# Optimization experiments

Measured on AMD Instinct MI355X. Metric: run time of the kernel, lower is better.

## Reference

```python
import jax, jax.numpy as jnp
import numpy as np

EPS = 1e-5
NEIGHBOR_K = 3
NEG_SLOPE = 0.2

def _conv(x, w):
    # x: [N,C,H,W], w: [O,I,3,3], stride 1, SAME padding
    return jax.lax.conv_general_dilated(
        x, w, window_strides=(1, 1), padding='SAME',
        dimension_numbers=('NCHW', 'OIHW', 'NCHW'))

def _bn(x, gamma, beta):
    # BatchNorm2d in training mode: batch statistics over (N,H,W), biased var
    m = x.mean(axis=(0, 2, 3), keepdims=True)
    v = x.var(axis=(0, 2, 3), keepdims=True)
    xn = (x - m) * jax.lax.rsqrt(v + EPS)
    return xn * gamma.reshape(1, -1, 1, 1) + beta.reshape(1, -1, 1, 1)

def _lrelu(x):
    return jnp.where(x >= 0, x, NEG_SLOPE * x)

def _maxpool2(x):
    return jax.lax.reduce_window(x, -jnp.inf, jax.lax.max,
                                 (1, 1, 2, 2), (1, 1, 2, 2), 'VALID')

def _features(x, w1, g1, b1, w2, g2, b2, w3, g3, b3, w4, g4, b4):
    x = _maxpool2(_lrelu(_bn(_conv(x, w1), g1, b1)))
    x = _maxpool2(_lrelu(_bn(_conv(x, w2), g2, b2)))
    x = _lrelu(_bn(_conv(x, w3), g3, b3))
    x = _lrelu(_bn(_conv(x, w4), g4, b4))
    return x  # [N, 64, 21, 21]

def setup_inputs() -> dict:
    key = jax.random.key(0)
    ks = jax.random.split(key, 8)
    inp = {
        'input1': jax.random.normal(ks[0], (32, 3, 84, 84), jnp.float32),
        'input2': jax.random.normal(ks[1], (5, 5, 3, 84, 84), jnp.float32),
        'w1': jax.random.normal(ks[2], (64, 3, 3, 3), jnp.float32) * 0.1,
        'g1': jax.random.uniform(ks[3], (64,), jnp.float32, 0.5, 1.5),
        'b1': jnp.zeros((64,), jnp.float32),
        'w2': jax.random.normal(ks[4], (64, 64, 3, 3), jnp.float32) * 0.1,
        'g2': jax.random.uniform(ks[5], (64,), jnp.float32, 0.5, 1.5),
        'b2': jnp.zeros((64,), jnp.float32),
        'w3': jax.random.normal(ks[6], (64, 64, 3, 3), jnp.float32) * 0.1,
        'g3': jax.random.uniform(ks[7], (64,), jnp.float32, 0.5, 1.5),
        'b3': jnp.zeros((64,), jnp.float32),
        'w4': jax.random.normal(jax.random.fold_in(key, 100), (64, 64, 3, 3), jnp.float32) * 0.1,
        'g4': jax.random.uniform(jax.random.fold_in(key, 101), (64,), jnp.float32, 0.5, 1.5),
        'b4': jnp.zeros((64,), jnp.float32),
    }
    return inp

def reference(input1, input2, w1, g1, b1, w2, g2, b2, w3, g3, b3, w4, g4, b4):
    params = (w1, g1, b1, w2, g2, b2, w3, g3, b3, w4, g4, b4)
    # Query features: [B, C, h, w]
    q = _features(input1, *params)
    B, C, h, w = q.shape
    hw = h * w
    Q = q.reshape(B, C, hw).transpose(0, 2, 1)            # [B, hw, C]
    qn = jnp.linalg.norm(Q, axis=2, keepdims=True)        # [B, hw, 1]
    # Support features, BN stats per class-batch (matches per-class forward)
    s = jax.vmap(lambda x: _features(x, *params))(input2) # [nc, shot, C, h, w]
    nc, shot = s.shape[0], s.shape[1]
    S = s.transpose(0, 2, 1, 3, 4).reshape(nc, C, shot * hw)  # [nc, C, M]
    sn = jnp.linalg.norm(S, axis=1, keepdims=True)            # [nc, 1, M]
    # Cosine similarities: [B, nc, hw, M]
    sims = jnp.einsum('bqc,ncm->bnqm', Q, S)
    sims = sims / (qn[:, None, :, :] * sn[None, :, :, :])
    topv = jax.lax.top_k(sims, NEIGHBOR_K)[0]              # [B, nc, hw, k]
    return topv.sum(axis=(2, 3))                           # [B, nc]
```

## Files before the change

kernel.cpp:

```cpp
#include <hip/hip_runtime.h>
#include <hip/hip_bf16.h>
#include <stdint.h>

#define NQ 32
#define NCLS 5
#define SHOT 5
#define NIMG 57
#define P1 7056
#define P2 1764
#define P3 441
#define PX 3528
#define MM (SHOT*P3)
#define EPSB 1e-5f
#define SLOPE 0.2f
#define NEGINF -3.4e38f
#define NREP 32
#define MSPAN 576
#define MRNG 4
#define SLS 88

typedef __attribute__((ext_vector_type(8))) short short8;
typedef __attribute__((ext_vector_type(4))) float f32x4;

__device__ inline float ldf(const float* p) { return *p; }
__device__ inline float ldf(const __hip_bfloat16* p) { return __bfloat162float(*p); }
__device__ inline void stf(float* p, float v) { *p = v; }
__device__ inline void stf(__hip_bfloat16* p, float v) { *p = __float2bfloat16(v); }

__device__ __forceinline__ unsigned short bf16bits(float v)
{
    __hip_bfloat16 h = __float2bfloat16(v);
    return *reinterpret_cast<unsigned short*>(&h);
}
__device__ __forceinline__ float bits2f(unsigned short u)
{
    unsigned int x = ((unsigned int)u) << 16;
    return *reinterpret_cast<float*>(&x);
}

__global__ void pack_all_k(const float* __restrict__ w1, const float* __restrict__ w2,
                           const float* __restrict__ w3, const float* __restrict__ w4,
                           unsigned short* __restrict__ wpk1, unsigned short* __restrict__ wpk2,
                           unsigned short* __restrict__ wpk3, unsigned short* __restrict__ wpk4,
                           float* __restrict__ sums)
{
    int i = blockIdx.x * 256 + threadIdx.x;
    if (i < 4 * 6 * 64 * 2 * NREP) sums[i] = 0.f;
    if (i < 3 * 36864) {
        int set = i / 36864, ii = i - set * 36864;
        const float* w = (set == 0) ? w2 : (set == 1) ? w3 : w4;
        unsigned short* wpk = (set == 0) ? wpk2 : (set == 1) ? wpk3 : wpk4;
        int j = ii & 7, lane = (ii >> 3) & 63, chunk = ii >> 9;
        int nt = chunk & 3, half = (chunk >> 2) & 1, t = chunk >> 3;
        int co = nt * 16 + (lane & 15);
        int ci = half * 32 + (lane >> 4) * 8 + j;
        wpk[ii] = bf16bits(w[co * 576 + ci * 9 + t]);
    } else {
        int ii = i - 3 * 36864;
        if (ii >= 4096) return;
        int j = ii & 7, lane = (ii >> 3) & 63, c8 = ii >> 9;
        int nt = c8 & 3, f = c8 >> 2;
        int co = nt * 16 + (lane & 15), q = lane >> 4;
        int k = q * 8 + j;
        float val = 0.f;
        if (f == 0) {
            int t = k >> 2, ci = k & 3;
            if (ci < 3) val = w1[co * 27 + ci * 9 + t];
        } else if (k < 4) {
            int ci = k & 3;
            if (ci < 3) val = w1[co * 27 + ci * 9 + 8];
        }
        wpk1[ii] = bf16bits(val);
    }
}

__global__ __launch_bounds__(256) void conv1m_k(const float* __restrict__ in1,
                                                const float* __restrict__ in2,
                                                const unsigned short* __restrict__ wpk1,
                                                __hip_bfloat16* __restrict__ xpool,
                                                float* __restrict__ sums)
{
    constexpr int S = 84, P = P1, MBLK = 256, NB = 28, SPAN = MBLK + 2 * S + 2;
    __shared__ __align__(16) unsigned short ls4[SPAN * 4];
    __shared__ float qs[4][64], qs2[4][64];
    int img = blockIdx.x / NB;
    int p0 = (blockIdx.x % NB) * MBLK;
    int tid = threadIdx.x, lane = tid & 63, wv = tid >> 6;
    int col = lane & 15, quad = lane >> 4;
    const float* in = (img < NQ) ? in1 + (size_t)img * 3 * P1
                                 : in2 + (size_t)(img - NQ) * 3 * P1;
    for (int u = tid; u < SPAN; u += 256) {
        int p = p0 - S - 1 + u;
        union { unsigned short us[4]; uint2 u2; } o;
        o.u2 = (uint2){0u, 0u};
        if (p >= 0 && p < P) {
            o.us[0] = bf16bits(in[p]);
            o.us[1] = bf16bits(in[P1 + p]);
            o.us[2] = bf16bits(in[2 * P1 + p]);
        }
        *(uint2*)(ls4 + u * 4) = o.u2;
    }
    const short8* wb = (const short8*)wpk1;
    short8 b0[4], b1[4];
    #pragma unroll
    for (int nt = 0; nt < 4; ++nt) {
        b0[nt] = wb[(size_t)(nt * 64 + lane)];
        b1[nt] = wb[(size_t)((4 + nt) * 64 + lane)];
    }
    int t0 = 2 * quad, t1 = t0 + 1;
    int d0 = (t0 / 3 - 1) * S + (t0 % 3 - 1);
    int d1 = (t1 / 3 - 1) * S + (t1 % 3 - 1);
    const int d8 = S + 1;
    int tx0 = t0 % 3, tx1 = t1 % 3;
    __syncthreads();
    f32x4 acc[4][4];
    #pragma unroll
    for (int mt = 0; mt < 4; ++mt)
        #pragma unroll
        for (int nt = 0; nt < 4; ++nt) acc[mt][nt] = (f32x4){0.f, 0.f, 0.f, 0.f};
    #pragma unroll
    for (int mt = 0; mt < 4; ++mt) {
        int pl = wv * 64 + mt * 16 + col;
        int xm = (p0 + pl) % S;
        int base = pl + S + 1;
        uint2 h0 = *(const uint2*)(ls4 + (base + d0) * 4);
        uint2 h1 = *(const uint2*)(ls4 + (base + d1) * 4);
        uint2 h8 = *(const uint2*)(ls4 + (base + d8) * 4);
        bool ok0 = (tx0 == 0) ? (xm >= 1) : ((tx0 == 2) ? (xm <= S - 2) : true);
        bool ok1 = (tx1 == 0) ? (xm >= 1) : ((tx1 == 2) ? (xm <= S - 2) : true);
        bool ok8 = (quad == 0) && (xm <= S - 2);
        if (!ok0) h0 = (uint2){0u, 0u};
        if (!ok1) h1 = (uint2){0u, 0u};
        if (!ok8) h8 = (uint2){0u, 0u};
        union { uint4 u; short8 s; } ca, cb;
        ca.u = (uint4){h0.x, h0.y, h1.x, h1.y};
        cb.u = (uint4){h8.x, h8.y, 0u, 0u};
        #pragma unroll
        for (int nt = 0; nt < 4; ++nt) {
            acc[mt][nt] = __builtin_amdgcn_mfma_f32_16x16x32_bf16(ca.s, b0[nt], acc[mt][nt], 0, 0, 0);
            acc[mt][nt] = __builtin_amdgcn_mfma_f32_16x16x32_bf16(cb.s, b1[nt], acc[mt][nt], 0, 0, 0);
        }
    }
    float s[4] = {0.f, 0.f, 0.f, 0.f}, s2[4] = {0.f, 0.f, 0.f, 0.f};
    __hip_bfloat16* ob = xpool + (size_t)img * PX * 64;
    #pragma unroll
    for (int mt = 0; mt < 4; ++mt) {
        int tb = p0 + wv * 64 + mt * 16 + quad * 4;
        #pragma unroll
        for (int reg = 0; reg < 4; ++reg) {
            int pr = tb + reg;
            if (pr < P) {
                #pragma unroll
                for (int nt = 0; nt < 4; ++nt) {
                    float v = acc[mt][nt][reg];
                    s[nt] += v;
                    s2[nt] = fmaf(v, v, s2[nt]);
                }
            }
        }
        #pragma unroll
        for (int pr2 = 0; pr2 < 2; ++pr2) {
            int m0 = tb + pr2 * 2;
            if (m0 < P) {
                #pragma unroll
                for (int nt = 0; nt < 4; ++nt) {
                    float v = fmaxf(acc[mt][nt][pr2 * 2], acc[mt][nt][pr2 * 2 + 1]);
                    ob[(size_t)(m0 >> 1) * 64 + nt * 16 + col] = __float2bfloat16(v);
                }
            }
        }
    }
    #pragma unroll
    for (int d = 16; d < 64; d <<= 1)
        #pragma unroll
        for (int nt = 0; nt < 4; ++nt) {
            s[nt] += __shfl_xor(s[nt], d, 64);
            s2[nt] += __shfl_xor(s2[nt], d, 64);
        }
    if (quad == 0) {
        #pragma unroll
        for (int nt = 0; nt < 4; ++nt) {
            qs[wv][nt * 16 + col] = s[nt];
            qs2[wv][nt * 16 + col] = s2[nt];
        }
    }
    __syncthreads();
    if (wv == 0) {
        int g = (img < NQ) ? 0 : 1 + (img - NQ) / SHOT;
        int rep = blockIdx.x & (NREP - 1);
        float ts = qs[0][lane] + qs[1][lane] + qs[2][lane] + qs[3][lane];
        float ts2 = qs2[0][lane] + qs2[1][lane] + qs2[2][lane] + qs2[3][lane];
        float* base = sums + ((size_t)(g * 64 + lane) * 2) * NREP + rep;
        atomicAdd(base, ts);
        atomicAdd(base + NREP, ts2);
    }
}

__global__ __launch_bounds__(256) void bnpooly_k(const unsigned short* __restrict__ in,
                                                 const float* __restrict__ ms,
                                                 unsigned short* __restrict__ out)
{
    int i = blockIdx.x * 256 + threadIdx.x;
    if (i >= NIMG * P2 * 16) return;
    int q4 = i & 15;
    int t = i >> 4;
    int p = t % P2;
    int img = t / P2;
    int y = p / 42, x2 = p - y * 42;
    int g = (img < NQ) ? 0 : 1 + (img - NQ) / SHOT;
    size_t base = ((size_t)img * PX + (size_t)(2 * y) * 42 + x2) * 16 + q4;
    ushort4 r0 = ((const ushort4*)in)[base];
    ushort4 r1 = ((const ushort4*)in)[base + 42 * 16];
    unsigned short a0[4] = {r0.x, r0.y, r0.z, r0.w};
    unsigned short a1[4] = {r1.x, r1.y, r1.z, r1.w};
    ushort4 o;
    unsigned short* os = (unsigned short*)&o;
    #pragma unroll
    for (int k = 0; k < 4; ++k) {
        int c = q4 * 4 + k;
        float v = fmaxf(bits2f(a0[k]), bits2f(a1[k]));
        v = fmaf(v, ms[(g * 64 + c) * 2], ms[(g * 64 + c) * 2 + 1]);
        v = fmaxf(v, SLOPE * v);
        os[k] = bf16bits(v);
    }
    ((ushort4*)out)[i] = o;
}

template <int S, int MBLK, bool BNIN, typename OT>
__global__ __launch_bounds__(256) void conv64m_k(const void* __restrict__ inv,
                                                 const unsigned short* __restrict__ wpk,
                                                 OT* __restrict__ out,
                                                 float* __restrict__ sums,
                                                 const float* __restrict__ msin)
{
    constexpr int P = S * S;
    constexpr int MT = MBLK / 64;
    constexpr int NB = (P + MBLK - 1) / MBLK;
    constexpr int SPAN = MBLK + 2 * S + 2;
    __shared__ __align__(16) unsigned short ls[SPAN * 72];
    __shared__ float qs[4][64], qs2[4][64];
    int img = blockIdx.x / NB;
    int p0 = (blockIdx.x % NB) * MBLK;
    int tid = threadIdx.x;
    int lane = tid & 63, wv = tid >> 6;
    int col = lane & 15, quad = lane >> 4;
    int g = (img < NQ) ? 0 : 1 + (img - NQ) / SHOT;
    if constexpr (!BNIN) {
        const unsigned short* ib = (const unsigned short*)inv + (size_t)img * P * 64;
        for (int u = tid; u < SPAN * 8; u += 256) {
            int pix = u >> 3, part = u & 7;
            int p = p0 - S - 1 + pix;
            short8 v = {0, 0, 0, 0, 0, 0, 0, 0};
            if (p >= 0 && p < P) v = *(const short8*)(ib + (size_t)p * 64 + part * 8);
            *(short8*)(ls + pix * 72 + part * 8) = v;
        }
    } else {
        const float* ib = (const float*)inv + (size_t)img * P * 64;
        int part = tid & 7;
        float ba[8], bb[8];
        #pragma unroll
        for (int j = 0; j < 8; ++j) {
            float2 ab = ((const float2*)msin)[g * 64 + part * 8 + j];
            ba[j] = ab.x;
            bb[j] = ab.y;
        }
        for (int u = tid; u < SPAN * 8; u += 256) {
            int pix = u >> 3;
            int p = p0 - S - 1 + pix;
            union { unsigned short us[8]; short8 s8; } o;
            #pragma unroll
            for (int j = 0; j < 8; ++j) o.us[j] = 0;
            if (p >= 0 && p < P) {
                const float* src = ib + (size_t)p * 64 + part * 8;
                float4 x0 = *(const float4*)src;
                float4 x1 = *(const float4*)(src + 4);
                float xs[8] = {x0.x, x0.y, x0.z, x0.w, x1.x, x1.y, x1.z, x1.w};
                #pragma unroll
                for (int j = 0; j < 8; ++j) {
                    float v = fmaf(xs[j], ba[j], bb[j]);
                    v = fmaxf(v, SLOPE * v);
                    o.us[j] = bf16bits(v);
                }
            }
            *(short8*)(ls + pix * 72 + part * 8) = o.s8;
        }
    }
    __syncthreads();
    f32x4 acc[MT][4];
    #pragma unroll
    for (int mt = 0; mt < MT; ++mt)
        #pragma unroll
        for (int nt = 0; nt < 4; ++nt) acc[mt][nt] = (f32x4){0.f, 0.f, 0.f, 0.f};
    bool mok0[MT], mok2[MT];
    #pragma unroll
    for (int mt = 0; mt < MT; ++mt) {
        int xm = (p0 + wv * (MT * 16) + mt * 16 + col) % S;
        mok0[mt] = xm >= 1;
        mok2[mt] = xm <= S - 2;
    }
    const short8* wb = (const short8*)wpk;
    #pragma unroll
    for (int ky = 0; ky < 3; ++ky) {
        #pragma unroll
        for (int kx = 0; kx < 3; ++kx) {
            int t = ky * 3 + kx;
            int d = (ky - 1) * S + (kx - 1);
            #pragma unroll
            for (int half = 0; half < 2; ++half) {
                short8 b[4];
                #pragma unroll
                for (int nt = 0; nt < 4; ++nt)
                    b[nt] = wb[((t * 2 + half) * 4 + nt) * 64 + lane];
                #pragma unroll
                for (int mt = 0; mt < MT; ++mt) {
                    int idx = wv * (MT * 16) + mt * 16 + col + S + 1 + d;
                    short8 a = *(const short8*)(ls + idx * 72 + half * 32 + quad * 8);
                    bool ok = (kx == 0) ? mok0[mt] : (kx == 2) ? mok2[mt] : true;
                    if (!ok) a = (short8){0, 0, 0, 0, 0, 0, 0, 0};
                    #pragma unroll
                    for (int nt = 0; nt < 4; ++nt)
                        acc[mt][nt] = __builtin_amdgcn_mfma_f32_16x16x32_bf16(a, b[nt], acc[mt][nt], 0, 0, 0);
                }
            }
        }
    }
    float s[4] = {0.f, 0.f, 0.f, 0.f}, s2[4] = {0.f, 0.f, 0.f, 0.f};
    OT* ob = out + (size_t)img * P * 64;
    #pragma unroll
    for (int mt = 0; mt < MT; ++mt) {
        int tb = p0 + wv * (MT * 16) + mt * 16 + quad * 4;
        #pragma unroll
        for (int reg = 0; reg < 4; ++reg) {
            int pr = tb + reg;
            if (pr < P) {
                #pragma unroll
                for (int nt = 0; nt < 4; ++nt) {
                    float v = acc[mt][nt][reg];
                    stf(ob + (size_t)pr * 64 + nt * 16 + col, v);
                    s[nt] += v;
                    s2[nt] = fmaf(v, v, s2[nt]);
                }
            }
        }
    }
    #pragma unroll
    for (int d = 16; d < 64; d <<= 1)
        #pragma unroll
        for (int nt = 0; nt < 4; ++nt) {
            s[nt] += __shfl_xor(s[nt], d, 64);
            s2[nt] += __shfl_xor(s2[nt], d, 64);
        }
    if (quad == 0) {
        #pragma unroll
        for (int nt = 0; nt < 4; ++nt) {
            qs[wv][nt * 16 + col] = s[nt];
            qs2[wv][nt * 16 + col] = s2[nt];
        }
    }
    __syncthreads();
    if (wv == 0) {
        int rep = blockIdx.x & (NREP - 1);
        float ts = qs[0][lane] + qs[1][lane] + qs[2][lane] + qs[3][lane];
        float ts2 = qs2[0][lane] + qs2[1][lane] + qs2[2][lane] + qs2[3][lane];
        float* base = sums + ((size_t)(g * 64 + lane) * 2) * NREP + rep;
        atomicAdd(base, ts);
        atomicAdd(base + NREP, ts2);
    }
}

__global__ void finalize_k(const float* __restrict__ sums, float* __restrict__ ms,
                           const float* __restrict__ gamma, const float* __restrict__ beta, int P)
{
    int i = blockIdx.x * blockDim.x + threadIdx.x;
    if (i >= 6 * 64) return;
    int g = i >> 6, c = i & 63;
    const float* ps = sums + (size_t)i * 2 * NREP;
    float s = 0.f, s2 = 0.f;
    #pragma unroll
    for (int r = 0; r < NREP; ++r) { s += ps[r]; s2 += ps[NREP + r]; }
    float cnt = (float)((g == 0 ? NQ : SHOT) * P);
    float mean = s / cnt;
    float var = s2 / cnt - mean * mean;
    float a = rsqrtf(var + EPSB) * gamma[c];
    ms[i * 2] = a;
    ms[i * 2 + 1] = fmaf(-mean, a, beta[c]);
}

template <typename T>
__global__ __launch_bounds__(256) void bnpool_k(const T* __restrict__ x, const float* __restrict__ ms,
                                                __hip_bfloat16* __restrict__ out, int Win)
{
    int Wout = Win >> 1, Pout = Wout * Wout;
    size_t idx = (size_t)blockIdx.x * 256 + threadIdx.x;
    size_t total = (size_t)NIMG * Pout * 64;
    if (idx >= total) return;
    int c = (int)(idx & 63);
    size_t t = idx >> 6;
    int p = (int)(t % Pout);
    int img = (int)(t / Pout);
    int y = p / Wout, xo = p - y * Wout;
    int g = (img < NQ) ? 0 : 1 + (img - NQ) / SHOT;
    float a = ms[(g * 64 + c) * 2], bb = ms[(g * 64 + c) * 2 + 1];
    const T* base = x + (((size_t)img * Win + 2 * y) * Win + 2 * xo) * 64 + c;
    float mx = -3.4e38f;
    #pragma unroll
    for (int dy = 0; dy < 2; ++dy)
        #pragma unroll
        for (int dx = 0; dx < 2; ++dx) {
            float v = ldf(base + ((size_t)dy * Win + dx) * 64);
            v = fmaf(v, a, bb);
            v = v >= 0.f ? v : SLOPE * v;
            mx = fmaxf(mx, v);
        }
    out[idx] = __float2bfloat16(mx);
}

__global__ __launch_bounds__(256) void bnnorm_k(const float* __restrict__ x, const float* __restrict__ ms,
                                                __hip_bfloat16* __restrict__ out)
{
    int lane = threadIdx.x & 63, wvr = threadIdx.x >> 6;
    int pix = blockIdx.x * 4 + wvr;
    if (pix >= NIMG * P3) return;
    int img = pix / P3;
    int g = (img < NQ) ? 0 : 1 + (img - NQ) / SHOT;
    float v = fmaf(x[(size_t)pix * 64 + lane], ms[(g * 64 + lane) * 2], ms[(g * 64 + lane) * 2 + 1]);
    v = v >= 0.f ? v : SLOPE * v;
    float ss = v * v;
    #pragma unroll
    for (int d = 32; d > 0; d >>= 1) ss += __shfl_xor(ss, d, 64);
    out[(size_t)pix * 64 + lane] = __float2bfloat16(v * rsqrtf(ss));
}

__device__ __forceinline__ void ins3(float v, float& t0, float& t1, float& t2)
{
    float n1 = __builtin_amdgcn_fmed3f(v, t0, t1);
    float n2 = __builtin_amdgcn_fmed3f(v, t1, t2);
    t0 = fmaxf(t0, v);
    t1 = n1;
    t2 = n2;
}

__global__ __launch_bounds__(256, 6) void sim_part_k(const __hip_bfloat16* __restrict__ fhat,
                                                     float* __restrict__ part)
{
    __shared__ __align__(16) unsigned short sl[64 * SLS];
    int t = blockIdx.x;
    int mr = t & 3;
    int qb = (t >> 2) % 7;
    int n = (t / 28) % NCLS;
    int bq = t / (28 * NCLS);
    int tid = threadIdx.x, lane = tid & 63, wv = tid >> 6;
    int col = lane & 15, quad = lane >> 4;
    int q = qb * 64 + wv * 16 + col;
    int qc = q < P3 ? q : P3 - 1;
    const unsigned short* qp = (const unsigned short*)fhat + ((size_t)bq * P3 + qc) * 64;
    short8 a0 = *(const short8*)(qp + quad * 8);
    short8 a1 = *(const short8*)(qp + 32 + quad * 8);
    const unsigned short* sp = (const unsigned short*)fhat + (size_t)(NQ + n * SHOT) * P3 * 64;
    int m_lo = mr * MSPAN;
    int m_cnt = MM - m_lo; if (m_cnt > MSPAN) m_cnt = MSPAN;
    int nch = (m_cnt + 63) >> 6;
    float t0[4], t1[4], t2[4];
    #pragma unroll
    for (int r = 0; r < 4; ++r) { t0[r] = NEGINF; t1[r] = NEGINF; t2[r] = NEGINF; }
    int srow = tid >> 3, scc = (tid & 7) * 8;
    for (int c = 0; c < nch; ++c) {
        int m0 = m_lo + c * 64;
        __syncthreads();
        #pragma unroll
        for (int pass = 0; pass < 2; ++pass) {
            int row = srow + pass * 32;
            int m = m0 + row;
            short8 vv = {0, 0, 0, 0, 0, 0, 0, 0};
            if (m < MM) vv = *(const short8*)(sp + (size_t)m * 64 + scc);
            *(short8*)(sl + row * SLS + scc) = vv;
        }
        __syncthreads();
        const unsigned short* sr = sl + col * SLS + quad * 8;
        #pragma unroll
        for (int mt = 0; mt < 4; ++mt) {
            if (m0 + mt * 16 < MM) {
                short8 b0 = *(const short8*)(sr);
                short8 b1 = *(const short8*)(sr + 32);
                f32x4 acc = {0.f, 0.f, 0.f, 0.f};
                acc = __builtin_amdgcn_mfma_f32_16x16x32_bf16(a0, b0, acc, 0, 0, 0);
                acc = __builtin_amdgcn_mfma_f32_16x16x32_bf16(a1, b1, acc, 0, 0, 0);
                #pragma unroll
                for (int r = 0; r < 4; ++r) ins3(acc[r], t0[r], t1[r], t2[r]);
            }
            sr += 16 * SLS;
        }
    }
    #pragma unroll
    for (int d = 1; d < 16; d <<= 1)
        #pragma unroll
        for (int r = 0; r < 4; ++r) {
            float u0 = __shfl_xor(t0[r], d, 64);
            float u1 = __shfl_xor(t1[r], d, 64);
            float u2 = __shfl_xor(t2[r], d, 64);
            ins3(u0, t0[r], t1[r], t2[r]);
            ins3(u1, t0[r], t1[r], t2[r]);
            ins3(u2, t0[r], t1[r], t2[r]);
        }
    if (col == 0) {
        #pragma unroll
        for (int r = 0; r < 4; ++r) {
            int ql = wv * 16 + quad * 4 + r;
            float* pp = part + ((((size_t)(bq * NCLS + n) * 7 + qb) * 4 + mr) * 64 + ql) * 3;
            pp[0] = t0[r];
            pp[1] = t1[r];
            pp[2] = t2[r];
        }
    }
}

__global__ __launch_bounds__(256) void sim_merge_k(const float* __restrict__ part,
                                                   float* __restrict__ out)
{
    __shared__ float red[4];
    int b = blockIdx.x;
    int tid = threadIdx.x, lane = tid & 63, wv = tid >> 6;
    float s = 0.f;
    for (int q = tid; q < P3; q += 256) {
        int qb = q >> 6, ql = q & 63;
        const float* pp = part + (((size_t)b * 7 + qb) * 4 * 64 + ql) * 3;
        float v0 = pp[0], v1 = pp[1], v2 = pp[2];
        #pragma unroll
        for (int mr = 1; mr < 4; ++mr) {
            const float* pm = pp + (size_t)mr * 192;
            ins3(pm[0], v0, v1, v2);
            ins3(pm[1], v0, v1, v2);
            ins3(pm[2], v0, v1, v2);
        }
        s += v0 + v1 + v2;
    }
    #pragma unroll
    for (int d = 32; d > 0; d >>= 1) s += __shfl_xor(s, d, 64);
    if (lane == 0) red[wv] = s;
    __syncthreads();
    if (tid == 0) out[b] = red[0] + red[1] + red[2] + red[3];
}

extern "C" void kernel_launch(void* const* d_in, const int* in_sizes, int n_in,
                              void* d_out, int out_size, void* d_ws, size_t ws_size,
                              hipStream_t stream)
{
    const float* input1 = (const float*)d_in[0];
    const float* input2 = (const float*)d_in[1];
    const float* w1 = (const float*)d_in[2];
    const float* g1 = (const float*)d_in[3];
    const float* b1 = (const float*)d_in[4];
    const float* w2 = (const float*)d_in[5];
    const float* g2 = (const float*)d_in[6];
    const float* b2 = (const float*)d_in[7];
    const float* w3 = (const float*)d_in[8];
    const float* g3 = (const float*)d_in[9];
    const float* b3 = (const float*)d_in[10];
    const float* w4 = (const float*)d_in[11];
    const float* g4 = (const float*)d_in[12];
    const float* b4 = (const float*)d_in[13];
    float* out = (float*)d_out;

    char* w8 = (char*)d_ws;
    const size_t oB = 51480576;
    const size_t oT = oB + 12870144;
    const size_t STG = 6 * 64 * 2 * NREP * sizeof(float);
    __hip_bfloat16* xpool = (__hip_bfloat16*)(w8 + 0);
    __hip_bfloat16* conv2raw = (__hip_bfloat16*)(w8 + 0);
    float* conv3raw = (float*)(w8 + 0);
    float* conv4raw = (float*)(w8 + 9652608);
    __hip_bfloat16* fhat = (__hip_bfloat16*)(w8 + 16087680);
    __hip_bfloat16* pooled1 = (__hip_bfloat16*)(w8 + oB);
    __hip_bfloat16* pooled2 = (__hip_bfloat16*)(w8 + oB);
    float* sums = (float*)(w8 + oT);
    float* ms = (float*)(w8 + oT + 4 * STG);
    unsigned short* wpk2 = (unsigned short*)(w8 + oT + 4 * STG + 12288);
    unsigned short* wpk3 = (unsigned short*)(w8 + oT + 4 * STG + 12288 + 73728);
    unsigned short* wpk4 = (unsigned short*)(w8 + oT + 4 * STG + 12288 + 147456);
    unsigned short* wpk1 = (unsigned short*)(w8 + oT + 4 * STG + 12288 + 221184);
    const size_t oP = oT + 4 * STG + 12288 + 221184 + 8192;
    float* part = (float*)(w8 + oP);
    if (ws_size < oP + (size_t)NQ * NCLS * 7 * MRNG * 64 * 3 * sizeof(float)) return;
    float* sums1 = sums;
    float* sums2 = sums + 6 * 64 * 2 * NREP;
    float* sums3 = sums2 + 6 * 64 * 2 * NREP;
    float* sums4 = sums3 + 6 * 64 * 2 * NREP;

    pack_all_k<<<448, 256, 0, stream>>>(w1, w2, w3, w4, wpk1, wpk2, wpk3, wpk4, sums);

    conv1m_k<<<NIMG * 28, 256, 0, stream>>>(input1, input2, wpk1, xpool, sums1);
    finalize_k<<<2, 256, 0, stream>>>(sums1, ms + 0, g1, b1, P1);
    bnpooly_k<<<(NIMG * P2 * 16 + 255) / 256, 256, 0, stream>>>(
        (const unsigned short*)xpool, ms + 0, (unsigned short*)pooled1);
    conv64m_k<42, 256, false, __hip_bfloat16><<<NIMG * 7, 256, 0, stream>>>(
        pooled1, wpk2, conv2raw, sums2, nullptr);
    finalize_k<<<2, 256, 0, stream>>>(sums2, ms + 768, g2, b2, P2);
    bnpool_k<__hip_bfloat16><<<6285, 256, 0, stream>>>(conv2raw, ms + 768, pooled2, 42);
    conv64m_k<21, 128, false, float><<<NIMG * 4, 256, 0, stream>>>(
        pooled2, wpk3, conv3raw, sums3, nullptr);
    finalize_k<<<2, 256, 0, stream>>>(sums3, ms + 1536, g3, b3, P3);
    conv64m_k<21, 128, true, float><<<NIMG * 4, 256, 0, stream>>>(
        conv3raw, wpk4, conv4raw, sums4, ms + 1536);
    finalize_k<<<2, 256, 0, stream>>>(sums4, ms + 2304, g4, b4, P3);
    bnnorm_k<<<6285, 256, 0, stream>>>(conv4raw, ms + 2304, fhat);
    sim_part_k<<<NQ * NCLS * 7 * MRNG, 256, 0, stream>>>(fhat, part);
    sim_merge_k<<<NQ * NCLS, 256, 0, stream>>>(part, out);
}
```

Measured before the change: 234.6 us.

## Fuse horizontal max-pool into conv2 epilogue and store conv3/conv4 outputs as bf16

```diff
diff --git a/kernel.cpp b/kernel.cpp
--- a/kernel.cpp
+++ b/kernel.cpp
@@ -21,11 +21,6 @@
 
 typedef __attribute__((ext_vector_type(8))) short short8;
 typedef __attribute__((ext_vector_type(4))) float f32x4;
-
-__device__ inline float ldf(const float* p) { return *p; }
-__device__ inline float ldf(const __hip_bfloat16* p) { return __bfloat162float(*p); }
-__device__ inline void stf(float* p, float v) { *p = v; }
-__device__ inline void stf(__hip_bfloat16* p, float v) { *p = __float2bfloat16(v); }
 
 __device__ __forceinline__ unsigned short bf16bits(float v)
 {
@@ -196,21 +191,23 @@
     }
 }
 
+template <int W>
 __global__ __launch_bounds__(256) void bnpooly_k(const unsigned short* __restrict__ in,
                                                  const float* __restrict__ ms,
                                                  unsigned short* __restrict__ out)
 {
+    constexpr int POUT = W * W;
     int i = blockIdx.x * 256 + threadIdx.x;
-    if (i >= NIMG * P2 * 16) return;
+    if (i >= NIMG * POUT * 16) return;
     int q4 = i & 15;
     int t = i >> 4;
-    int p = t % P2;
-    int img = t / P2;
-    int y = p / 42, x2 = p - y * 42;
+    int p = t % POUT;
+    int img = t / POUT;
+    int y = p / W, x2 = p - y * W;
     int g = (img < NQ) ? 0 : 1 + (img - NQ) / SHOT;
-    size_t base = ((size_t)img * PX + (size_t)(2 * y) * 42 + x2) * 16 + q4;
+    size_t base = ((size_t)img * (2 * POUT) + (size_t)(2 * y) * W + x2) * 16 + q4;
     ushort4 r0 = ((const ushort4*)in)[base];
-    ushort4 r1 = ((const ushort4*)in)[base + 42 * 16];
+    ushort4 r1 = ((const ushort4*)in)[base + W * 16];
     unsigned short a0[4] = {r0.x, r0.y, r0.z, r0.w};
     unsigned short a1[4] = {r1.x, r1.y, r1.z, r1.w};
     ushort4 o;
@@ -226,10 +223,10 @@
     ((ushort4*)out)[i] = o;
 }
 
-template <int S, int MBLK, bool BNIN, typename OT>
-__global__ __launch_bounds__(256) void conv64m_k(const void* __restrict__ inv,
+template <int S, int MBLK, bool BNIN, bool POOLX>
+__global__ __launch_bounds__(256) void conv64m_k(const unsigned short* __restrict__ inv,
                                                  const unsigned short* __restrict__ wpk,
-                                                 OT* __restrict__ out,
+                                                 __hip_bfloat16* __restrict__ out,
                                                  float* __restrict__ sums,
                                                  const float* __restrict__ msin)
 {
@@ -245,8 +242,8 @@
     int lane = tid & 63, wv = tid >> 6;
     int col = lane & 15, quad = lane >> 4;
     int g = (img < NQ) ? 0 : 1 + (img - NQ) / SHOT;
+    const unsigned short* ib = inv + (size_t)img * P * 64;
     if constexpr (!BNIN) {
-        const unsigned short* ib = (const unsigned short*)inv + (size_t)img * P * 64;
         for (int u = tid; u < SPAN * 8; u += 256) {
             int pix = u >> 3, part = u & 7;
             int p = p0 - S - 1 + pix;
@@ -255,7 +252,6 @@
             *(short8*)(ls + pix * 72 + part * 8) = v;
         }
     } else {
-        const float* ib = (const float*)inv + (size_t)img * P * 64;
         int part = tid & 7;
         float ba[8], bb[8];
         #pragma unroll
@@ -271,13 +267,11 @@
             #pragma unroll
             for (int j = 0; j < 8; ++j) o.us[j] = 0;
             if (p >= 0 && p < P) {
-                const float* src = ib + (size_t)p * 64 + part * 8;
-                float4 x0 = *(const float4*)src;
-                float4 x1 = *(const float4*)(src + 4);
-                float xs[8] = {x0.x, x0.y, x0.z, x0.w, x1.x, x1.y, x1.z, x1.w};
+                union { short8 s8; unsigned short us[8]; } x;
+                x.s8 = *(const short8*)(ib + (size_t)p * 64 + part * 8);
                 #pragma unroll
                 for (int j = 0; j < 8; ++j) {
-                    float v = fmaf(xs[j], ba[j], bb[j]);
+                    float v = fmaf(bits2f(x.us[j]), ba[j], bb[j]);
                     v = fmaxf(v, SLOPE * v);
                     o.us[j] = bf16bits(v);
                 }
@@ -325,7 +319,7 @@
         }
     }
     float s[4] = {0.f, 0.f, 0.f, 0.f}, s2[4] = {0.f, 0.f, 0.f, 0.f};
-    OT* ob = out + (size_t)img * P * 64;
+    __hip_bfloat16* ob = out + (size_t)img * (POOLX ? P / 2 : P) * 64;
     #pragma unroll
     for (int mt = 0; mt < MT; ++mt) {
         int tb = p0 + wv * (MT * 16) + mt * 16 + quad * 4;
@@ -336,9 +330,31 @@
                 #pragma unroll
                 for (int nt = 0; nt < 4; ++nt) {
                     float v = acc[mt][nt][reg];
-                    stf(ob + (size_t)pr * 64 + nt * 16 + col, v);
                     s[nt] += v;
                     s2[nt] = fmaf(v, v, s2[nt]);
+                }
+            }
+        }
+        if constexpr (POOLX) {
+            #pragma unroll
+            for (int pr2 = 0; pr2 < 2; ++pr2) {
+                int m0 = tb + pr2 * 2;
+                if (m0 < P) {
+                    #pragma unroll
+                    for (int nt = 0; nt < 4; ++nt) {
+                        float v = fmaxf(acc[mt][nt][pr2 * 2], acc[mt][nt][pr2 * 2 + 1]);
+                        ob[(size_t)(m0 >> 1) * 64 + nt * 16 + col] = __float2bfloat16(v);
+                    }
+                }
+            }
+        } else {
+            #pragma unroll
+            for (int reg = 0; reg < 4; ++reg) {
+                int pr = tb + reg;
+                if (pr < P) {
+                    #pragma unroll
+                    for (int nt = 0; nt < 4; ++nt)
+                        ob[(size_t)pr * 64 + nt * 16 + col] = __float2bfloat16(acc[mt][nt][reg]);
                 }
             }
         }
@@ -386,36 +402,8 @@
     ms[i * 2 + 1] = fmaf(-mean, a, beta[c]);
 }
 
-template <typename T>
-__global__ __launch_bounds__(256) void bnpool_k(const T* __restrict__ x, const float* __restrict__ ms,
-                                                __hip_bfloat16* __restrict__ out, int Win)
-{
-    int Wout = Win >> 1, Pout = Wout * Wout;
-    size_t idx = (size_t)blockIdx.x * 256 + threadIdx.x;
-    size_t total = (size_t)NIMG * Pout * 64;
-    if (idx >= total) return;
-    int c = (int)(idx & 63);
-    size_t t = idx >> 6;
-    int p = (int)(t % Pout);
-    int img = (int)(t / Pout);
-    int y = p / Wout, xo = p - y * Wout;
-    int g = (img < NQ) ? 0 : 1 + (img - NQ) / SHOT;
-    float a = ms[(g * 64 + c) * 2], bb = ms[(g * 64 + c) * 2 + 1];
-    const T* base = x + (((size_t)img * Win + 2 * y) * Win + 2 * xo) * 64 + c;
-    float mx = -3.4e38f;
-    #pragma unroll
-    for (int dy = 0; dy < 2; ++dy)
-        #pragma unroll
-        for (int dx = 0; dx < 2; ++dx) {
-            float v = ldf(base + ((size_t)dy * Win + dx) * 64);
-            v = fmaf(v, a, bb);
-            v = v >= 0.f ? v : SLOPE * v;
-            mx = fmaxf(mx, v);
-        }
-    out[idx] = __float2bfloat16(mx);
-}
-
-__global__ __launch_bounds__(256) void bnnorm_k(const float* __restrict__ x, const float* __restrict__ ms,
+__global__ __launch_bounds__(256) void bnnorm_k(const unsigned short* __restrict__ x,
+                                                const float* __restrict__ ms,
                                                 __hip_bfloat16* __restrict__ out)
 {
     int lane = threadIdx.x & 63, wvr = threadIdx.x >> 6;
@@ -423,7 +411,7 @@
     if (pix >= NIMG * P3) return;
     int img = pix / P3;
     int g = (img < NQ) ? 0 : 1 + (img - NQ) / SHOT;
-    float v = fmaf(x[(size_t)pix * 64 + lane], ms[(g * 64 + lane) * 2], ms[(g * 64 + lane) * 2 + 1]);
+    float v = fmaf(bits2f(x[(size_t)pix * 64 + lane]), ms[(g * 64 + lane) * 2], ms[(g * 64 + lane) * 2 + 1]);
     v = v >= 0.f ? v : SLOPE * v;
     float ss = v * v;
     #pragma unroll
@@ -566,9 +554,9 @@
     const size_t oT = oB + 12870144;
     const size_t STG = 6 * 64 * 2 * NREP * sizeof(float);
     __hip_bfloat16* xpool = (__hip_bfloat16*)(w8 + 0);
-    __hip_bfloat16* conv2raw = (__hip_bfloat16*)(w8 + 0);
-    float* conv3raw = (float*)(w8 + 0);
-    float* conv4raw = (float*)(w8 + 9652608);
+    __hip_bfloat16* xpool2 = (__hip_bfloat16*)(w8 + 0);
+    __hip_bfloat16* conv3raw = (__hip_bfloat16*)(w8 + 0);
+    __hip_bfloat16* conv4raw = (__hip_bfloat16*)(w8 + 9652608);
     __hip_bfloat16* fhat = (__hip_bfloat16*)(w8 + 16087680);
     __hip_bfloat16* pooled1 = (__hip_bfloat16*)(w8 + oB);
     __hip_bfloat16* pooled2 = (__hip_bfloat16*)(w8 + oB);
@@ -590,19 +578,20 @@
 
     conv1m_k<<<NIMG * 28, 256, 0, stream>>>(input1, input2, wpk1, xpool, sums1);
     finalize_k<<<2, 256, 0, stream>>>(sums1, ms + 0, g1, b1, P1);
-    bnpooly_k<<<(NIMG * P2 * 16 + 255) / 256, 256, 0, stream>>>(
+    bnpooly_k<42><<<(NIMG * P2 * 16 + 255) / 256, 256, 0, stream>>>(
         (const unsigned short*)xpool, ms + 0, (unsigned short*)pooled1);
-    conv64m_k<42, 256, false, __hip_bfloat16><<<NIMG * 7, 256, 0, stream>>>(
-        pooled1, wpk2, conv2raw, sums2, nullptr);
+    conv64m_k<42, 256, false, true><<<NIMG * 7, 256, 0, stream>>>(
+        (const unsigned short*)pooled1, wpk2, xpool2, sums2, nullptr);
     finalize_k<<<2, 256, 0, stream>>>(sums2, ms + 768, g2, b2, P2);
-    bnpool_k<__hip_bfloat16><<<6285, 256, 0, stream>>>(conv2raw, ms + 768, pooled2, 42);
-    conv64m_k<21, 128, false, float><<<NIMG * 4, 256, 0, stream>>>(
-        pooled2, wpk3, conv3raw, sums3, nullptr);
+    bnpooly_k<21><<<(NIMG * P3 * 16 + 255) / 256, 256, 0, stream>>>(
+        (const unsigned short*)xpool2, ms + 768, (unsigned short*)pooled2);
+    conv64m_k<21, 128, false, false><<<NIMG * 4, 256, 0, stream>>>(
+        (const unsigned short*)pooled2, wpk3, conv3raw, sums3, nullptr);
     finalize_k<<<2, 256, 0, stream>>>(sums3, ms + 1536, g3, b3, P3);
-    conv64m_k<21, 128, true, float><<<NIMG * 4, 256, 0, stream>>>(
-        conv3raw, wpk4, conv4raw, sums4, ms + 1536);
+    conv64m_k<21, 128, true, false><<<NIMG * 4, 256, 0, stream>>>(
+        (const unsigned short*)conv3raw, wpk4, conv4raw, sums4, ms + 1536);
     finalize_k<<<2, 256, 0, stream>>>(sums4, ms + 2304, g4, b4, P3);
-    bnnorm_k<<<6285, 256, 0, stream>>>(conv4raw, ms + 2304, fhat);
+    bnnorm_k<<<6285, 256, 0, stream>>>((const unsigned short*)conv4raw, ms + 2304, fhat);
     sim_part_k<<<NQ * NCLS * 7 * MRNG, 256, 0, stream>>>(fhat, part);
     sim_merge_k<<<NQ * NCLS, 256, 0, stream>>>(part, out);
 }
```

Measured after the change: 231.4 us. No clear change (-1.4%).
